# Kernel optimization log

Hardware: AMD Instinct MI355X
Metric: run time of the kernel (lower is better)

## Reference

```python
import jax, jax.numpy as jnp
import numpy as np
from jax import lax

G = 128          # graphs per batch
N_PER = 512      # nodes per graph (uniform -> static top-k shapes)
N = G * N_PER    # 65536 total nodes
E = 1_048_576    # total edges (8192 per graph)
IN, D, OUT = 256, 128, 16
BN_EPS = 1e-5


def setup_inputs() -> dict:
    key = jax.random.key(0)
    ks = jax.random.split(key, 20)
    e_per = E // G
    off = (jnp.arange(G, dtype=jnp.int32) * N_PER)[:, None]
    src = (off + jax.random.randint(ks[0], (G, e_per), 0, N_PER, dtype=jnp.int32)).reshape(-1)
    dst = (off + jax.random.randint(ks[1], (G, e_per), 0, N_PER, dtype=jnp.int32)).reshape(-1)
    inp = {
        "x": jax.random.normal(ks[2], (N, IN), dtype=jnp.float32),
        "edge_index": jnp.stack([src, dst]),
        "batch": jnp.repeat(jnp.arange(G, dtype=jnp.int32), N_PER),
        # GraphConv1: lin_rel (with bias) + lin_root (no bias)
        "w_rel1": jax.random.normal(ks[3], (IN, D)) / np.sqrt(IN),
        "b_rel1": jnp.zeros((D,), jnp.float32),
        "w_root1": jax.random.normal(ks[4], (IN, D)) / np.sqrt(IN),
        "pool1_w": jax.random.normal(ks[5], (D,)) / np.sqrt(D),
        "w_rel2": jax.random.normal(ks[6], (D, D)) / np.sqrt(D),
        "b_rel2": jnp.zeros((D,), jnp.float32),
        "w_root2": jax.random.normal(ks[7], (D, D)) / np.sqrt(D),
        "pool2_w": jax.random.normal(ks[8], (D,)) / np.sqrt(D),
        "lin1_w": jax.random.normal(ks[9], (2 * D, D)) / np.sqrt(2 * D),
        "lin1_b": jnp.zeros((D,), jnp.float32),
        "bn_gamma": jnp.ones((D,), jnp.float32),
        "bn_beta": jnp.zeros((D,), jnp.float32),
        "bn_mean": jnp.zeros((D,), jnp.float32),
        "bn_var": jnp.ones((D,), jnp.float32),
        "lin2_w": jax.random.normal(ks[10], (D, OUT)) / np.sqrt(D),
        "lin2_b": jnp.zeros((OUT,), jnp.float32),
    }
    return inp


def _graph_conv(x, src, dst, valid, w_rel, b_rel, w_root):
    # PyG GraphConv (aggr='add'): lin_rel(sum_{j in N(i)} x_j) + lin_root(x_i)
    msgs = jnp.where(valid[:, None], x[src], 0.0)           # [E, F]
    agg = jax.ops.segment_sum(msgs, dst, num_segments=x.shape[0])
    return agg @ w_rel + b_rel + x @ w_root


def _topk_pool(x, src, dst, valid, w, n_per):
    # PyG TopKPooling: score = sigmoid(x.w / ||w||); keep top ceil(ratio*n) per graph
    k = (n_per + 1) // 2  # ceil(0.5 * n_per)
    score = jax.nn.sigmoid((x @ w) / jnp.sqrt(jnp.sum(w * w)))  # [G*n_per]
    idx_local = lax.top_k(score.reshape(G, n_per), k)[1]        # [G, k]
    perm = (jnp.arange(G, dtype=src.dtype)[:, None] * n_per + idx_local.astype(src.dtype)).reshape(-1)
    x_new = x[perm] * score[perm][:, None]
    # relabel edges (filter_adj): keep edges with both endpoints selected
    mapping = jnp.full((G * n_per,), -1, dtype=src.dtype).at[perm].set(
        jnp.arange(G * k, dtype=src.dtype))
    ns, nd = mapping[src], mapping[dst]
    v = valid & (ns >= 0) & (nd >= 0)
    return x_new, jnp.where(v, ns, 0), jnp.where(v, nd, 0), v, score[perm], k


def _global_pools(x, k):
    xg = x.reshape(G, k, -1)
    return jnp.concatenate([xg.max(axis=1), xg.mean(axis=1)], axis=1)  # [G, 2D]


def reference(x, edge_index, batch, w_rel1, b_rel1, w_root1, pool1_w,
              w_rel2, b_rel2, w_root2, pool2_w, lin1_w, lin1_b,
              bn_gamma, bn_beta, bn_mean, bn_var, lin2_w, lin2_b):
    src, dst = edge_index[0], edge_index[1]
    valid = jnp.ones_like(src, dtype=bool)

    h = jax.nn.relu(_graph_conv(x, src, dst, valid, w_rel1, b_rel1, w_root1))
    h, s1, d1, v1, score_1, k1 = _topk_pool(h, src, dst, valid, pool1_w, N_PER)
    x1 = _global_pools(h, k1)

    h = jax.nn.relu(_graph_conv(h, s1, d1, v1, w_rel2, b_rel2, w_root2))
    h, _, _, _, _, k2 = _topk_pool(h, s1, d1, v1, pool2_w, k1)
    x2 = _global_pools(h, k2)

    g_emb = x1 + x2                                  # [G, 2D]
    z = jax.nn.relu(g_emb @ lin1_w + lin1_b)
    z = (z - bn_mean) * bn_gamma / jnp.sqrt(bn_var + BN_EPS) + bn_beta  # BN (eval)
    # dropout is identity in eval mode
    out = jax.nn.log_softmax(z @ lin2_w + lin2_b, axis=-1)
    return out, g_emb, pool1_w, score_1
```

## Files before the change

### kernel.cpp

```cpp
#include <hip/hip_runtime.h>
#include <cmath>

#define NG    128
#define NPER  512
#define NTOT  65536
#define NEDGE 1048576
#define EPG   8192
#define DD    128
#define K1    256
#define K2    128
#define SLOTS 56

typedef float f32x4 __attribute__((ext_vector_type(4)));
typedef short short8 __attribute__((ext_vector_type(8)));

__device__ __forceinline__ int SW(int row, int c) { return (c ^ ((row >> 1) & 3)) * 8; }

__device__ __forceinline__ void bsplit(float v, short& h, short& l) {
  unsigned u = __builtin_bit_cast(unsigned, v);
  h = (short)(u >> 16);
  float lf = v - __builtin_bit_cast(float, u & 0xFFFF0000u);
  l = (short)(__builtin_bit_cast(unsigned, lf) >> 16);
}

__device__ __forceinline__ void gload16(const void* g, void* l) {
  __builtin_amdgcn_global_load_lds(
      (const __attribute__((address_space(1))) unsigned int*)g,
      (__attribute__((address_space(3))) unsigned int*)l, 16, 0, 0);
}

__global__ __launch_bounds__(256) void build_wt_all(
    const float* __restrict__ W1, const float* __restrict__ W2,
    const float* __restrict__ W3, const float* __restrict__ W4,
    short* __restrict__ h1, short* __restrict__ l1,
    short* __restrict__ h2, short* __restrict__ l2, int* __restrict__ cnt) {
  const int n = blockIdx.x, k = threadIdx.x;
  cnt[n * 256 + k] = 0;
  const int t = k >> 5, k5 = k & 31, cq = k5 >> 3, i = k5 & 7;
  const int nhalf = n >> 7, nf = (n >> 4) & 7, l = n & 15;
  const int off = ((((t * 2 + nhalf) * 8 + nf) * 4 + cq) * 16 + l) * 8 + i;
  {
    float w = (nhalf == 0) ? W1[k * 128 + n] : W2[k * 128 + (n - 128)];
    short h, lo; bsplit(w, h, lo);
    h1[off] = h; l1[off] = lo;
  }
  if (k < 128) {
    float w = (nhalf == 0) ? W3[k * 128 + n] : W4[k * 128 + (n - 128)];
    short h, lo; bsplit(w, h, lo);
    h2[off] = h; l2[off] = lo;
  }
}

template<int K>
__global__ __launch_bounds__(256, 4) void gemm_mfma_dual(
    const float* __restrict__ A,
    const short* __restrict__ wth, const short* __restrict__ wtl,
    float* __restrict__ C1, float* __restrict__ C2) {
  __shared__ short Ah[64 * 32], Al[64 * 32];
  __shared__ short WHL[16384];
  const int tid = threadIdx.x, lane = tid & 63, wid = tid >> 6;
  const int wm = (wid >> 1) * 32;
  const int nhalf = wid & 1;
  const size_t row0 = (size_t)blockIdx.x * 64;
  const int l15 = lane & 15, cq = lane >> 4;
  const int ar = tid >> 2, ac = tid & 3;
  constexpr int NT = K / 32;
  const float* ap = A + (row0 + ar) * K + ac * 8;
  const int wfrag = nhalf * 4096 + cq * 128 + l15 * 8;

  f32x4 acc[2][8];
#pragma unroll
  for (int mf = 0; mf < 2; ++mf)
#pragma unroll
    for (int nf = 0; nf < 8; ++nf) acc[mf][nf] = (f32x4){0.f, 0.f, 0.f, 0.f};

  float4 pa0, pa1;
#define LOAD_A(t) { const float4* p = (const float4*)(ap + (t) * 32); pa0 = p[0]; pa1 = p[1]; }
#define STORE_A() { \
    float ff[8] = {pa0.x, pa0.y, pa0.z, pa0.w, pa1.x, pa1.y, pa1.z, pa1.w}; \
    short8 hv, lv; \
    _Pragma("unroll") \
    for (int i = 0; i < 8; ++i) { short hh, ll; bsplit(ff[i], hh, ll); hv[i] = hh; lv[i] = ll; } \
    *(short8*)&Ah[ar * 32 + SW(ar, ac)] = hv; \
    *(short8*)&Al[ar * 32 + SW(ar, ac)] = lv; }
#define STAGE_W(t) { \
    _Pragma("unroll") \
    for (int j = 0; j < 8; ++j) { \
      int c = wid * 8 + j; \
      const short* gs = (c < 16) ? wth + (size_t)(t) * 8192 + c * 512 + lane * 8 \
                                 : wtl + (size_t)(t) * 8192 + (c - 16) * 512 + lane * 8; \
      gload16(gs, &WHL[c * 512 + lane * 8]); \
    } }

  LOAD_A(0);
  STAGE_W(0);
  STORE_A();
  __syncthreads();

  for (int t = 0; t < NT; ++t) {
    if (t + 1 < NT) LOAD_A(t + 1);
    const int r0 = wm + l15, r1 = wm + 16 + l15;
    short8 ah0 = *(const short8*)&Ah[r0 * 32 + SW(r0, cq)];
    short8 al0 = *(const short8*)&Al[r0 * 32 + SW(r0, cq)];
    short8 ah1 = *(const short8*)&Ah[r1 * 32 + SW(r1, cq)];
    short8 al1 = *(const short8*)&Al[r1 * 32 + SW(r1, cq)];
#pragma unroll
    for (int nf = 0; nf < 8; ++nf) {
      short8 bh = *(const short8*)&WHL[nf * 512 + wfrag];
      short8 bl = *(const short8*)&WHL[8192 + nf * 512 + wfrag];
      acc[0][nf] = __builtin_amdgcn_mfma_f32_16x16x32_bf16(ah0, bh, acc[0][nf], 0, 0, 0);
      acc[0][nf] = __builtin_amdgcn_mfma_f32_16x16x32_bf16(ah0, bl, acc[0][nf], 0, 0, 0);
      acc[0][nf] = __builtin_amdgcn_mfma_f32_16x16x32_bf16(al0, bh, acc[0][nf], 0, 0, 0);
      acc[1][nf] = __builtin_amdgcn_mfma_f32_16x16x32_bf16(ah1, bh, acc[1][nf], 0, 0, 0);
      acc[1][nf] = __builtin_amdgcn_mfma_f32_16x16x32_bf16(ah1, bl, acc[1][nf], 0, 0, 0);
      acc[1][nf] = __builtin_amdgcn_mfma_f32_16x16x32_bf16(al1, bh, acc[1][nf], 0, 0, 0);
    }
    if (t + 1 < NT) {
      __syncthreads();
      STAGE_W(t + 1);
      STORE_A();
      __syncthreads();
    }
  }
#undef LOAD_A
#undef STORE_A
#undef STAGE_W

  float* Cb = nhalf ? C2 : C1;
#pragma unroll
  for (int mf = 0; mf < 2; ++mf) {
    size_t rbase = row0 + wm + mf * 16 + cq * 4;
#pragma unroll
    for (int nf = 0; nf < 8; ++nf) {
      int c = nf * 16 + l15;
#pragma unroll
      for (int r = 0; r < 4; ++r)
        Cb[(rbase + r) * 128 + c] = acc[mf][nf][r];
    }
  }
}

__global__ __launch_bounds__(512) void bucket_fill1(
    const int* __restrict__ src, const int* __restrict__ dst,
    int* __restrict__ cnt, int* __restrict__ eid) {
  int e = blockIdx.x * 512 + threadIdx.x;
  int d = dst[e];
  int pos = atomicAdd(&cnt[d], 1);
  eid[d * SLOTS + pos] = src[e];
}

__global__ __launch_bounds__(512) void bucket_fill2(
    const int* __restrict__ src, const int* __restrict__ dst,
    const int* __restrict__ map, int* __restrict__ cnt, int* __restrict__ eid) {
  int e = blockIdx.x * 512 + threadIdx.x;
  int ms = map[src[e]], md = map[dst[e]];
  if ((ms | md) >= 0) {
    int pos = atomicAdd(&cnt[md], 1);
    eid[md * SLOTS + pos] = ms;
  }
}

template<int CPX>
__global__ __launch_bounds__(512) void agg_gather(
    const float* __restrict__ xr, const float* __restrict__ xo,
    const float* __restrict__ brel, const int* __restrict__ cnt,
    const int* __restrict__ eid, const float* __restrict__ pw,
    float* __restrict__ hout, float* __restrict__ score) {
  const int bid = blockIdx.x;
  const int lb = (bid & 7) * CPX + (bid >> 3);
  const int wave = threadIdx.x >> 6, lane = threadIdx.x & 63;
  const int node = lb * 8 + wave;
  const int dg = cnt[node];
  const int base = node * SLOTS;
  const int half = lane >> 5, l32 = lane & 31;
  const int eall = eid[base + lane];
  f32x4 a0 = {0.f, 0.f, 0.f, 0.f}, a1 = a0, a2 = a0, a3 = a0;
  int j = 0;
  for (; j + 8 <= dg; j += 8) {
    int e0 = __shfl(eall, j + 0 + half);
    int e1 = __shfl(eall, j + 2 + half);
    int e2 = __shfl(eall, j + 4 + half);
    int e3 = __shfl(eall, j + 6 + half);
    a0 += *(const f32x4*)&xr[(size_t)e0 * 128 + l32 * 4];
    a1 += *(const f32x4*)&xr[(size_t)e1 * 128 + l32 * 4];
    a2 += *(const f32x4*)&xr[(size_t)e2 * 128 + l32 * 4];
    a3 += *(const f32x4*)&xr[(size_t)e3 * 128 + l32 * 4];
  }
  if (j + 4 <= dg) {
    int e0 = __shfl(eall, j + 0 + half);
    int e1 = __shfl(eall, j + 2 + half);
    a0 += *(const f32x4*)&xr[(size_t)e0 * 128 + l32 * 4];
    a1 += *(const f32x4*)&xr[(size_t)e1 * 128 + l32 * 4];
    j += 4;
  }
  if (j + 2 <= dg) {
    int e0 = __shfl(eall, j + half);
    a2 += *(const f32x4*)&xr[(size_t)e0 * 128 + l32 * 4];
    j += 2;
  }
  {
    int e0 = __shfl(eall, j);
    if (j < dg && half == 0)
      a3 += *(const f32x4*)&xr[(size_t)e0 * 128 + l32 * 4];
  }
  f32x4 s = a0 + a1 + a2 + a3;
  s[0] += __shfl_xor(s[0], 32);
  s[1] += __shfl_xor(s[1], 32);
  s[2] += __shfl_xor(s[2], 32);
  s[3] += __shfl_xor(s[3], 32);
  float dot = 0.f, nr = 0.f;
  if (half == 0) {
    f32x4 b = *(const f32x4*)&brel[l32 * 4];
    f32x4 o = *(const f32x4*)&xo[(size_t)node * 128 + l32 * 4];
    f32x4 h;
    f32x4 wv = *(const f32x4*)&pw[l32 * 4];
#pragma unroll
    for (int i = 0; i < 4; ++i) {
      h[i] = fmaxf(s[i] + b[i] + o[i], 0.f);
      dot += h[i] * wv[i];
      nr += wv[i] * wv[i];
    }
    *(f32x4*)&hout[(size_t)node * 128 + l32 * 4] = h;
  }
#pragma unroll
  for (int m = 16; m >= 1; m >>= 1) {
    dot += __shfl_xor(dot, m);
    nr += __shfl_xor(nr, m);
  }
  if (lane == 0)
    score[node] = 1.f / (1.f + expf(-dot / sqrtf(nr)));
}

__global__ __launch_bounds__(512) void topk1_kernel(
    const float* __restrict__ h1, const float* __restrict__ score_in,
    float* __restrict__ xnew, int* __restrict__ map, int* __restrict__ cnt,
    float* __restrict__ x1p, float* __restrict__ score_out) {
  const int g = blockIdx.x, tid = threadIdx.x;
  __shared__ float sc[NPER];
  __shared__ int si[NPER];
  __shared__ float xn[K1 * 128];
  __shared__ float redm[4 * 128];
  __shared__ float reds[4 * 128];
  {
    int gt = g * 512 + tid;
    if (gt < NG * K1) cnt[gt] = 0;
  }
  sc[tid] = score_in[g * NPER + tid];
  si[tid] = tid;

  for (int k = 2; k <= NPER; k <<= 1) {
    for (int j = k >> 1; j > 0; j >>= 1) {
      __syncthreads();
      int p = tid ^ j;
      if (p > tid) {
        float sa = sc[tid], sb = sc[p];
        int ia = si[tid], ib = si[p];
        bool before = (sb > sa) || (sb == sa && ib < ia);
        if (before == ((tid & k) == 0)) {
          sc[tid] = sb; sc[p] = sa; si[tid] = ib; si[p] = ia;
        }
      }
    }
  }
  __syncthreads();

  map[g * NPER + tid] = -1;
  if (tid < K1) score_out[g * K1 + tid] = sc[tid];
  __syncthreads();
  if (tid < K1) map[g * NPER + si[tid]] = g * K1 + tid;

  const int wave = tid >> 6, lane = tid & 63;
  for (int j = wave; j < K1; j += 8) {
    int idx = si[j];
    float s2 = sc[j];
    float2 v = *(const float2*)&h1[(size_t)(g * NPER + idx) * 128 + lane * 2];
    float2 o;
    o.x = v.x * s2;
    o.y = v.y * s2;
    *(float2*)&xnew[(size_t)(g * K1 + j) * 128 + lane * 2] = o;
    xn[j * 128 + lane * 2] = o.x;
    xn[j * 128 + lane * 2 + 1] = o.y;
  }
  __syncthreads();

  const int c = tid & 127, grp = tid >> 7;
  float mx = -1e30f, sm = 0.f;
  for (int r = grp; r < K1; r += 4) {
    float v = xn[r * 128 + c];
    mx = fmaxf(mx, v);
    sm += v;
  }
  redm[grp * 128 + c] = mx;
  reds[grp * 128 + c] = sm;
  __syncthreads();
  if (tid < 128) {
    float m = fmaxf(fmaxf(redm[c], redm[128 + c]), fmaxf(redm[256 + c], redm[384 + c]));
    float su = reds[c] + reds[128 + c] + reds[256 + c] + reds[384 + c];
    x1p[g * 256 + tid] = m;
    x1p[g * 256 + 128 + tid] = su * (1.f / 256.f);
  }
}

__global__ __launch_bounds__(256) void topk2_head_kernel(
    const float* __restrict__ h2, const float* __restrict__ score_in,
    const float* __restrict__ x1p,
    const float* __restrict__ lin1_w, const float* __restrict__ lin1_b,
    const float* __restrict__ bng, const float* __restrict__ bnb,
    const float* __restrict__ bnm, const float* __restrict__ bnv,
    const float* __restrict__ lin2_w, const float* __restrict__ lin2_b,
    const float* __restrict__ pool1_w, float* __restrict__ out) {
  const int g = blockIdx.x, tid = threadIdx.x;
  __shared__ float sc[K1];
  __shared__ int si[K1];
  __shared__ float xn[K2 * 128];
  __shared__ float redm[2 * 128];
  __shared__ float reds[2 * 128];
  __shared__ float ge[256];
  __shared__ float zz[128];
  __shared__ float lg[16];
  sc[tid] = score_in[g * K1 + tid];
  si[tid] = tid;
  for (int k = 2; k <= K1; k <<= 1) {
    for (int j = k >> 1; j > 0; j >>= 1) {
      __syncthreads();
      int p = tid ^ j;
      if (p > tid) {
        float sa = sc[tid], sb = sc[p];
        int ia = si[tid], ib = si[p];
        bool before = (sb > sa) || (sb == sa && ib < ia);
        if (before == ((tid & k) == 0)) {
          sc[tid] = sb; sc[p] = sa; si[tid] = ib; si[p] = ia;
        }
      }
    }
  }
  __syncthreads();
  const int wave = tid >> 6, lane = tid & 63;
  for (int j = wave; j < K2; j += 4) {
    int idx = si[j];
    float s2 = sc[j];
    float2 v = *(const float2*)&h2[(size_t)(g * K1 + idx) * 128 + lane * 2];
    xn[j * 128 + lane * 2] = v.x * s2;
    xn[j * 128 + lane * 2 + 1] = v.y * s2;
  }
  __syncthreads();
  const int c = tid & 127, grp = tid >> 7;
  float mx = -1e30f, sm = 0.f;
  for (int r = grp; r < K2; r += 2) {
    float v = xn[r * 128 + c];
    mx = fmaxf(mx, v);
    sm += v;
  }
  redm[grp * 128 + c] = mx;
  reds[grp * 128 + c] = sm;
  __syncthreads();
  if (tid < 128) {
    float m = fmaxf(redm[c], redm[128 + c]);
    float su = (reds[c] + reds[128 + c]) * (1.f / 128.f);
    float v1 = x1p[g * 256 + tid] + m;
    float v2 = x1p[g * 256 + 128 + tid] + su;
    ge[tid] = v1;
    ge[128 + tid] = v2;
    out[2048 + g * 256 + tid] = v1;
    out[2048 + g * 256 + 128 + tid] = v2;
  }
  __syncthreads();
  if (tid < 128) {
    float a = lin1_b[tid];
    for (int k = 0; k < 256; ++k) a += ge[k] * lin1_w[k * 128 + tid];
    a = fmaxf(a, 0.f);
    a = (a - bnm[tid]) * bng[tid] / sqrtf(bnv[tid] + 1e-5f) + bnb[tid];
    zz[tid] = a;
  }
  __syncthreads();
  if (tid < 16) {
    float o = lin2_b[tid];
    for (int k = 0; k < 128; ++k) o += zz[k] * lin2_w[k * 16 + tid];
    lg[tid] = o;
  }
  __syncthreads();
  if (tid < 16) {
    float m = lg[0];
    for (int j = 1; j < 16; ++j) m = fmaxf(m, lg[j]);
    float ssum = 0.f;
    for (int j = 0; j < 16; ++j) ssum += expf(lg[j] - m);
    out[g * 16 + tid] = lg[tid] - m - logf(ssum);
  }
  if (g == 0 && tid < 128) out[34816 + tid] = pool1_w[tid];
}

extern "C" void kernel_launch(void* const* d_in, const int* in_sizes, int n_in,
                              void* d_out, int out_size, void* d_ws, size_t ws_size,
                              hipStream_t stream) {
  const float* x       = (const float*)d_in[0];
  const int*   ei      = (const int*)d_in[1];
  const float* w_rel1  = (const float*)d_in[3];
  const float* b_rel1  = (const float*)d_in[4];
  const float* w_root1 = (const float*)d_in[5];
  const float* pool1_w = (const float*)d_in[6];
  const float* w_rel2  = (const float*)d_in[7];
  const float* b_rel2  = (const float*)d_in[8];
  const float* w_root2 = (const float*)d_in[9];
  const float* pool2_w = (const float*)d_in[10];
  const float* lin1_w  = (const float*)d_in[11];
  const float* lin1_b  = (const float*)d_in[12];
  const float* bng     = (const float*)d_in[13];
  const float* bnb     = (const float*)d_in[14];
  const float* bnm     = (const float*)d_in[15];
  const float* bnv     = (const float*)d_in[16];
  const float* lin2_w  = (const float*)d_in[17];
  const float* lin2_b  = (const float*)d_in[18];
  const int* src = ei;
  const int* dst = ei + NEDGE;

  char* ws = (char*)d_ws;
  float* xr1  = (float*)(ws + 0);
  float* xoh1 = (float*)(ws + 33554432UL);
  float* xnew = (float*)(ws + 67108864UL);
  int*   eid  = (int*)  (ws + 67108864UL);
  int*   map  = (int*)  (ws + 83886080UL);
  int*   cnt  = (int*)  (ws + 84148224UL);
  float* x1p  = (float*)(ws + 84410368UL);
  float* sc1  = (float*)(ws + 84541440UL);
  float* sc2  = (float*)(ws + 84803584UL);
  short* wth1 = (short*)(ws + 84934656UL);
  short* wtl1 = (short*)(ws + 85065728UL);
  short* wth2 = (short*)(ws + 85196800UL);
  short* wtl2 = (short*)(ws + 85262336UL);
  float* xr2  = (float*)(ws + 0);
  float* xo2  = (float*)(ws + 16777216UL);
  float* h2   = xoh1;
  float* out  = (float*)d_out;

  build_wt_all<<<dim3(256), dim3(256), 0, stream>>>(
      w_rel1, w_root1, w_rel2, w_root2, wth1, wtl1, wth2, wtl2, cnt);
  gemm_mfma_dual<256><<<dim3(1024), dim3(256), 0, stream>>>(x, wth1, wtl1, xr1, xoh1);
  bucket_fill1<<<dim3(NEDGE / 512), dim3(512), 0, stream>>>(src, dst, cnt, eid);
  agg_gather<1024><<<dim3(8192), dim3(512), 0, stream>>>(
      xr1, xoh1, b_rel1, cnt, eid, pool1_w, xoh1, sc1);
  topk1_kernel<<<dim3(NG), dim3(512), 0, stream>>>(xoh1, sc1, xnew, map, cnt, x1p, out + 34944);

  gemm_mfma_dual<128><<<dim3(512), dim3(256), 0, stream>>>(xnew, wth2, wtl2, xr2, xo2);
  bucket_fill2<<<dim3(NEDGE / 512), dim3(512), 0, stream>>>(src, dst, map, cnt, eid);
  agg_gather<512><<<dim3(4096), dim3(512), 0, stream>>>(
      xr2, xo2, b_rel2, cnt, eid, pool2_w, h2, sc2);

  topk2_head_kernel<<<dim3(NG), dim3(K1), 0, stream>>>(h2, sc2, x1p,
      lin1_w, lin1_b, bng, bnb, bnm, bnv, lin2_w, lin2_b, pool1_w, out);
}
```

Measured before the change: 183.8 us.

## Process eight nodes per wave in agg_gather with wider unroll and prefetch

Each wave in agg_gather now handles eight consecutive destination nodes instead of one. The grid shrinks eightfold, the pool-weight norm and bias loads are hoisted out of the node loop, and the next node's edge-id row is prefetched. The inner gather loop is unrolled to eight independent accumulators, and the tail uses clamped, predicated loads instead of a cascade of branches. The aim is to amortise per-node setup and raise memory-level parallelism per wave, at the cost of more registers (launch bounds now request 4 blocks) and fewer, longer-lived blocks, which can hurt load balance.

```diff
diff --git a/kernel.cpp b/kernel.cpp
--- a/kernel.cpp
+++ b/kernel.cpp
@@ -161,7 +161,7 @@
 }
 
 template<int CPX>
-__global__ __launch_bounds__(512) void agg_gather(
+__global__ __launch_bounds__(512, 4) void agg_gather(
     const float* __restrict__ xr, const float* __restrict__ xo,
     const float* __restrict__ brel, const int* __restrict__ cnt,
     const int* __restrict__ eid, const float* __restrict__ pw,
@@ -169,66 +169,83 @@
   const int bid = blockIdx.x;
   const int lb = (bid & 7) * CPX + (bid >> 3);
   const int wave = threadIdx.x >> 6, lane = threadIdx.x & 63;
-  const int node = lb * 8 + wave;
-  const int dg = cnt[node];
-  const int base = node * SLOTS;
   const int half = lane >> 5, l32 = lane & 31;
-  const int eall = eid[base + lane];
-  f32x4 a0 = {0.f, 0.f, 0.f, 0.f}, a1 = a0, a2 = a0, a3 = a0;
-  int j = 0;
-  for (; j + 8 <= dg; j += 8) {
-    int e0 = __shfl(eall, j + 0 + half);
-    int e1 = __shfl(eall, j + 2 + half);
-    int e2 = __shfl(eall, j + 4 + half);
-    int e3 = __shfl(eall, j + 6 + half);
-    a0 += *(const f32x4*)&xr[(size_t)e0 * 128 + l32 * 4];
-    a1 += *(const f32x4*)&xr[(size_t)e1 * 128 + l32 * 4];
-    a2 += *(const f32x4*)&xr[(size_t)e2 * 128 + l32 * 4];
-    a3 += *(const f32x4*)&xr[(size_t)e3 * 128 + l32 * 4];
-  }
-  if (j + 4 <= dg) {
-    int e0 = __shfl(eall, j + 0 + half);
-    int e1 = __shfl(eall, j + 2 + half);
-    a0 += *(const f32x4*)&xr[(size_t)e0 * 128 + l32 * 4];
-    a1 += *(const f32x4*)&xr[(size_t)e1 * 128 + l32 * 4];
-    j += 4;
-  }
-  if (j + 2 <= dg) {
-    int e0 = __shfl(eall, j + half);
-    a2 += *(const f32x4*)&xr[(size_t)e0 * 128 + l32 * 4];
-    j += 2;
-  }
-  {
-    int e0 = __shfl(eall, j);
-    if (j < dg && half == 0)
-      a3 += *(const f32x4*)&xr[(size_t)e0 * 128 + l32 * 4];
-  }
-  f32x4 s = a0 + a1 + a2 + a3;
-  s[0] += __shfl_xor(s[0], 32);
-  s[1] += __shfl_xor(s[1], 32);
-  s[2] += __shfl_xor(s[2], 32);
-  s[3] += __shfl_xor(s[3], 32);
-  float dot = 0.f, nr = 0.f;
-  if (half == 0) {
-    f32x4 b = *(const f32x4*)&brel[l32 * 4];
-    f32x4 o = *(const f32x4*)&xo[(size_t)node * 128 + l32 * 4];
+  const int n0 = lb * 64 + wave * 8;
+
+  const f32x4 wv = *(const f32x4*)&pw[l32 * 4];
+  float nr = wv[0] * wv[0] + wv[1] * wv[1] + wv[2] * wv[2] + wv[3] * wv[3];
+#pragma unroll
+  for (int m = 16; m >= 1; m >>= 1) nr += __shfl_xor(nr, m);
+  const float innorm = 1.f / sqrtf(nr);
+  const f32x4 bb = *(const f32x4*)&brel[l32 * 4];
+
+  int cnts = cnt[n0 + (lane & 7)];
+  int eall = eid[(size_t)n0 * SLOTS + lane];
+
+#define GLD(e) (*(const f32x4*)&xr[(size_t)(e) * 128 + l32 * 4])
+  for (int i = 0; i < 8; ++i) {
+    const int node = n0 + i;
+    const int dg = __shfl(cnts, i);
+    const int ecur = eall;
+    if (i < 7) eall = eid[(size_t)(node + 1) * SLOTS + lane];
+
+    f32x4 a0 = {0.f, 0.f, 0.f, 0.f}, a1 = a0, a2 = a0, a3 = a0,
+          a4 = a0, a5 = a0, a6 = a0, a7 = a0;
+    int j = 0;
+    for (; j + 16 <= dg; j += 16) {
+      int e0 = __shfl(ecur, j + 0 + half);
+      int e1 = __shfl(ecur, j + 2 + half);
+      int e2 = __shfl(ecur, j + 4 + half);
+      int e3 = __shfl(ecur, j + 6 + half);
+      int e4 = __shfl(ecur, j + 8 + half);
+      int e5 = __shfl(ecur, j + 10 + half);
+      int e6 = __shfl(ecur, j + 12 + half);
+      int e7 = __shfl(ecur, j + 14 + half);
+      a0 += GLD(e0); a1 += GLD(e1); a2 += GLD(e2); a3 += GLD(e3);
+      a4 += GLD(e4); a5 += GLD(e5); a6 += GLD(e6); a7 += GLD(e7);
+    }
+    if (j < dg) {
+      const int dm = dg - 1;
+      int i0 = j + 0 + half, i1 = j + 2 + half, i2 = j + 4 + half, i3 = j + 6 + half;
+      int i4 = j + 8 + half, i5 = j + 10 + half, i6 = j + 12 + half, i7 = j + 14 + half;
+      int e0 = __shfl(ecur, i0 < dm ? i0 : dm);
+      int e1 = __shfl(ecur, i1 < dm ? i1 : dm);
+      int e2 = __shfl(ecur, i2 < dm ? i2 : dm);
+      int e3 = __shfl(ecur, i3 < dm ? i3 : dm);
+      int e4 = __shfl(ecur, i4 < dm ? i4 : dm);
+      int e5 = __shfl(ecur, i5 < dm ? i5 : dm);
+      int e6 = __shfl(ecur, i6 < dm ? i6 : dm);
+      int e7 = __shfl(ecur, i7 < dm ? i7 : dm);
+      f32x4 v0 = GLD(e0), v1 = GLD(e1), v2 = GLD(e2), v3 = GLD(e3);
+      f32x4 v4 = GLD(e4), v5 = GLD(e5), v6 = GLD(e6), v7 = GLD(e7);
+      if (i0 <= dm) a0 += v0;
+      if (i1 <= dm) a1 += v1;
+      if (i2 <= dm) a2 += v2;
+      if (i3 <= dm) a3 += v3;
+      if (i4 <= dm) a4 += v4;
+      if (i5 <= dm) a5 += v5;
+      if (i6 <= dm) a6 += v6;
+      if (i7 <= dm) a7 += v7;
+    }
+    f32x4 s = ((a0 + a1) + (a2 + a3)) + ((a4 + a5) + (a6 + a7));
+    s[0] += __shfl_xor(s[0], 32);
+    s[1] += __shfl_xor(s[1], 32);
+    s[2] += __shfl_xor(s[2], 32);
+    s[3] += __shfl_xor(s[3], 32);
+    const f32x4 o = *(const f32x4*)&xo[(size_t)node * 128 + l32 * 4];
     f32x4 h;
-    f32x4 wv = *(const f32x4*)&pw[l32 * 4];
-#pragma unroll
-    for (int i = 0; i < 4; ++i) {
-      h[i] = fmaxf(s[i] + b[i] + o[i], 0.f);
-      dot += h[i] * wv[i];
-      nr += wv[i] * wv[i];
-    }
-    *(f32x4*)&hout[(size_t)node * 128 + l32 * 4] = h;
-  }
-#pragma unroll
-  for (int m = 16; m >= 1; m >>= 1) {
-    dot += __shfl_xor(dot, m);
-    nr += __shfl_xor(nr, m);
-  }
-  if (lane == 0)
-    score[node] = 1.f / (1.f + expf(-dot / sqrtf(nr)));
+    float dot = 0.f;
+#pragma unroll
+    for (int q = 0; q < 4; ++q) {
+      h[q] = fmaxf(s[q] + bb[q] + o[q], 0.f);
+      dot += h[q] * wv[q];
+    }
+    if (half == 0) *(f32x4*)&hout[(size_t)node * 128 + l32 * 4] = h;
+#pragma unroll
+    for (int m = 16; m >= 1; m >>= 1) dot += __shfl_xor(dot, m);
+    if (lane == 0) score[node] = 1.f / (1.f + expf(-dot * innorm));
+  }
+#undef GLD
 }
 
 __global__ __launch_bounds__(512) void topk1_kernel(
@@ -436,13 +453,13 @@
       w_rel1, w_root1, w_rel2, w_root2, wth1, wtl1, wth2, wtl2, cnt);
   gemm_mfma_dual<256><<<dim3(1024), dim3(256), 0, stream>>>(x, wth1, wtl1, xr1, xoh1);
   bucket_fill1<<<dim3(NEDGE / 512), dim3(512), 0, stream>>>(src, dst, cnt, eid);
-  agg_gather<1024><<<dim3(8192), dim3(512), 0, stream>>>(
+  agg_gather<128><<<dim3(1024), dim3(512), 0, stream>>>(
       xr1, xoh1, b_rel1, cnt, eid, pool1_w, xoh1, sc1);
   topk1_kernel<<<dim3(NG), dim3(512), 0, stream>>>(xoh1, sc1, xnew, map, cnt, x1p, out + 34944);
 
   gemm_mfma_dual<128><<<dim3(512), dim3(256), 0, stream>>>(xnew, wth2, wtl2, xr2, xo2);
   bucket_fill2<<<dim3(NEDGE / 512), dim3(512), 0, stream>>>(src, dst, map, cnt, eid);
-  agg_gather<512><<<dim3(4096), dim3(512), 0, stream>>>(
+  agg_gather<64><<<dim3(512), dim3(512), 0, stream>>>(
       xr2, xo2, b_rel2, cnt, eid, pool2_w, h2, sc2);
 
   topk2_head_kernel<<<dim3(NG), dim3(K1), 0, stream>>>(h2, sc2, x1p,
```

After: 195.1 us. +6.2%, slower.

## Stage per-graph features in LDS for neighbor aggregation and retile second GEMM

Applied to the files above, without the earlier changes.

Both aggregation kernels now give each block one graph (split into two feature or node halves). The block copies that graph's transformed features into shared memory and gathers neighbor rows from LDS instead of doing random global loads. Layer 1 accumulates a partial score dot product with atomics, and the sigmoid and norm move into topk1, which costs an extra memset. The second GEMM switches to 32-row tiles to launch more blocks. The trade-off is fewer, LDS-heavy blocks (256 per aggregation) with lower occupancy.

```diff
diff --git a/kernel.cpp b/kernel.cpp
--- a/kernel.cpp
+++ b/kernel.cpp
@@ -51,32 +51,34 @@
   }
 }
 
-template<int K>
+template<int K, int MT>
 __global__ __launch_bounds__(256, 4) void gemm_mfma_dual(
     const float* __restrict__ A,
     const short* __restrict__ wth, const short* __restrict__ wtl,
     float* __restrict__ C1, float* __restrict__ C2) {
-  __shared__ short Ah[64 * 32], Al[64 * 32];
+  constexpr int MF = MT / 32;
+  __shared__ short Ah[MT * 32], Al[MT * 32];
   __shared__ short WHL[16384];
   const int tid = threadIdx.x, lane = tid & 63, wid = tid >> 6;
-  const int wm = (wid >> 1) * 32;
+  const int wm = (wid >> 1) * (MT / 2);
   const int nhalf = wid & 1;
-  const size_t row0 = (size_t)blockIdx.x * 64;
+  const size_t row0 = (size_t)blockIdx.x * MT;
   const int l15 = lane & 15, cq = lane >> 4;
   const int ar = tid >> 2, ac = tid & 3;
+  const bool astage = (MT == 64) || (tid < MT * 4);
   constexpr int NT = K / 32;
   const float* ap = A + (row0 + ar) * K + ac * 8;
   const int wfrag = nhalf * 4096 + cq * 128 + l15 * 8;
 
-  f32x4 acc[2][8];
-#pragma unroll
-  for (int mf = 0; mf < 2; ++mf)
+  f32x4 acc[MF][8];
+#pragma unroll
+  for (int mf = 0; mf < MF; ++mf)
 #pragma unroll
     for (int nf = 0; nf < 8; ++nf) acc[mf][nf] = (f32x4){0.f, 0.f, 0.f, 0.f};
 
   float4 pa0, pa1;
-#define LOAD_A(t) { const float4* p = (const float4*)(ap + (t) * 32); pa0 = p[0]; pa1 = p[1]; }
-#define STORE_A() { \
+#define LOAD_A(t) if (astage) { const float4* p = (const float4*)(ap + (t) * 32); pa0 = p[0]; pa1 = p[1]; }
+#define STORE_A() if (astage) { \
     float ff[8] = {pa0.x, pa0.y, pa0.z, pa0.w, pa1.x, pa1.y, pa1.z, pa1.w}; \
     short8 hv, lv; \
     _Pragma("unroll") \
@@ -99,21 +101,23 @@
 
   for (int t = 0; t < NT; ++t) {
     if (t + 1 < NT) LOAD_A(t + 1);
-    const int r0 = wm + l15, r1 = wm + 16 + l15;
-    short8 ah0 = *(const short8*)&Ah[r0 * 32 + SW(r0, cq)];
-    short8 al0 = *(const short8*)&Al[r0 * 32 + SW(r0, cq)];
-    short8 ah1 = *(const short8*)&Ah[r1 * 32 + SW(r1, cq)];
-    short8 al1 = *(const short8*)&Al[r1 * 32 + SW(r1, cq)];
+    short8 ah[MF], al[MF];
+#pragma unroll
+    for (int mf = 0; mf < MF; ++mf) {
+      int r = wm + mf * 16 + l15;
+      ah[mf] = *(const short8*)&Ah[r * 32 + SW(r, cq)];
+      al[mf] = *(const short8*)&Al[r * 32 + SW(r, cq)];
+    }
 #pragma unroll
     for (int nf = 0; nf < 8; ++nf) {
       short8 bh = *(const short8*)&WHL[nf * 512 + wfrag];
       short8 bl = *(const short8*)&WHL[8192 + nf * 512 + wfrag];
-      acc[0][nf] = __builtin_amdgcn_mfma_f32_16x16x32_bf16(ah0, bh, acc[0][nf], 0, 0, 0);
-      acc[0][nf] = __builtin_amdgcn_mfma_f32_16x16x32_bf16(ah0, bl, acc[0][nf], 0, 0, 0);
-      acc[0][nf] = __builtin_amdgcn_mfma_f32_16x16x32_bf16(al0, bh, acc[0][nf], 0, 0, 0);
-      acc[1][nf] = __builtin_amdgcn_mfma_f32_16x16x32_bf16(ah1, bh, acc[1][nf], 0, 0, 0);
-      acc[1][nf] = __builtin_amdgcn_mfma_f32_16x16x32_bf16(ah1, bl, acc[1][nf], 0, 0, 0);
-      acc[1][nf] = __builtin_amdgcn_mfma_f32_16x16x32_bf16(al1, bh, acc[1][nf], 0, 0, 0);
+#pragma unroll
+      for (int mf = 0; mf < MF; ++mf) {
+        acc[mf][nf] = __builtin_amdgcn_mfma_f32_16x16x32_bf16(ah[mf], bh, acc[mf][nf], 0, 0, 0);
+        acc[mf][nf] = __builtin_amdgcn_mfma_f32_16x16x32_bf16(ah[mf], bl, acc[mf][nf], 0, 0, 0);
+        acc[mf][nf] = __builtin_amdgcn_mfma_f32_16x16x32_bf16(al[mf], bh, acc[mf][nf], 0, 0, 0);
+      }
     }
     if (t + 1 < NT) {
       __syncthreads();
@@ -128,7 +132,7 @@
 
   float* Cb = nhalf ? C2 : C1;
 #pragma unroll
-  for (int mf = 0; mf < 2; ++mf) {
+  for (int mf = 0; mf < MF; ++mf) {
     size_t rbase = row0 + wm + mf * 16 + cq * 4;
 #pragma unroll
     for (int nf = 0; nf < 8; ++nf) {
@@ -160,79 +164,140 @@
   }
 }
 
-template<int CPX>
-__global__ __launch_bounds__(512) void agg_gather(
+__global__ __launch_bounds__(512) void agg1_lds(
+    const float* __restrict__ xr, const float* __restrict__ xo,
+    const float* __restrict__ brel, const int* __restrict__ cnt,
+    const int* __restrict__ eid, const float* __restrict__ pw,
+    float* __restrict__ hout, float* __restrict__ sc_raw) {
+  __shared__ float Xs[512 * 68];
+  const int g = blockIdx.x >> 1, chunk = blockIdx.x & 1;
+  const int tid = threadIdx.x;
+  const int gn0 = g * NPER;
+  {
+    const float* srcp = xr + (size_t)gn0 * 128 + chunk * 64;
+#pragma unroll
+    for (int i = 0; i < 16; ++i) {
+      int fid = tid + i * 512;
+      int row = fid >> 4, q = fid & 15;
+      f32x4 v = *(const f32x4*)&srcp[(size_t)row * 128 + q * 4];
+      *(f32x4*)&Xs[row * 68 + q * 4] = v;
+    }
+  }
+  __syncthreads();
+  const int wave = tid >> 6, lane = tid & 63;
+  const int g4 = lane >> 4, c4 = (lane & 15) * 4;
+  const int nb = wave * 64;
+  const f32x4 wv = *(const f32x4*)&pw[chunk * 64 + c4];
+  const f32x4 bb = *(const f32x4*)&brel[chunk * 64 + c4];
+  int cnts = cnt[gn0 + nb + lane];
+  int eall = eid[(size_t)(gn0 + nb) * SLOTS + lane];
+  for (int i = 0; i < 64; ++i) {
+    const int node = gn0 + nb + i;
+    const int dg = __shfl(cnts, i);
+    const int ecur = eall;
+    if (i < 63) eall = eid[(size_t)(node + 1) * SLOTS + lane];
+    const int eoffv = (ecur - gn0) * 68;
+    f32x4 a = {0.f, 0.f, 0.f, 0.f};
+    int j = 0;
+    for (; j + 4 <= dg; j += 4) {
+      int ro = __shfl(eoffv, j + g4);
+      a += *(const f32x4*)&Xs[ro + c4];
+    }
+    if (j < dg) {
+      int sel = j + g4;
+      int ro = __shfl(eoffv, (sel < dg) ? sel : (dg - 1));
+      f32x4 v = *(const f32x4*)&Xs[ro + c4];
+      if (sel < dg) a += v;
+    }
+    a[0] += __shfl_xor(a[0], 16); a[1] += __shfl_xor(a[1], 16);
+    a[2] += __shfl_xor(a[2], 16); a[3] += __shfl_xor(a[3], 16);
+    a[0] += __shfl_xor(a[0], 32); a[1] += __shfl_xor(a[1], 32);
+    a[2] += __shfl_xor(a[2], 32); a[3] += __shfl_xor(a[3], 32);
+    float pd = 0.f;
+    if (g4 == 0) {
+      f32x4 o = *(const f32x4*)&xo[(size_t)node * 128 + chunk * 64 + c4];
+      f32x4 h;
+#pragma unroll
+      for (int q = 0; q < 4; ++q) {
+        h[q] = fmaxf(a[q] + bb[q] + o[q], 0.f);
+        pd += h[q] * wv[q];
+      }
+      *(f32x4*)&hout[(size_t)node * 128 + chunk * 64 + c4] = h;
+    }
+    pd += __shfl_xor(pd, 1); pd += __shfl_xor(pd, 2);
+    pd += __shfl_xor(pd, 4); pd += __shfl_xor(pd, 8);
+    if (lane == 0) atomicAdd(&sc_raw[node], pd);
+  }
+}
+
+__global__ __launch_bounds__(512) void agg2_lds(
     const float* __restrict__ xr, const float* __restrict__ xo,
     const float* __restrict__ brel, const int* __restrict__ cnt,
     const int* __restrict__ eid, const float* __restrict__ pw,
     float* __restrict__ hout, float* __restrict__ score) {
-  const int bid = blockIdx.x;
-  const int lb = (bid & 7) * CPX + (bid >> 3);
-  const int wave = threadIdx.x >> 6, lane = threadIdx.x & 63;
-  const int node = lb * 8 + wave;
-  const int dg = cnt[node];
-  const int base = node * SLOTS;
-  const int half = lane >> 5, l32 = lane & 31;
-  const int eall = eid[base + lane];
-  f32x4 a0 = {0.f, 0.f, 0.f, 0.f}, a1 = a0, a2 = a0, a3 = a0;
-  int j = 0;
-  for (; j + 8 <= dg; j += 8) {
-    int e0 = __shfl(eall, j + 0 + half);
-    int e1 = __shfl(eall, j + 2 + half);
-    int e2 = __shfl(eall, j + 4 + half);
-    int e3 = __shfl(eall, j + 6 + half);
-    a0 += *(const f32x4*)&xr[(size_t)e0 * 128 + l32 * 4];
-    a1 += *(const f32x4*)&xr[(size_t)e1 * 128 + l32 * 4];
-    a2 += *(const f32x4*)&xr[(size_t)e2 * 128 + l32 * 4];
-    a3 += *(const f32x4*)&xr[(size_t)e3 * 128 + l32 * 4];
-  }
-  if (j + 4 <= dg) {
-    int e0 = __shfl(eall, j + 0 + half);
-    int e1 = __shfl(eall, j + 2 + half);
-    a0 += *(const f32x4*)&xr[(size_t)e0 * 128 + l32 * 4];
-    a1 += *(const f32x4*)&xr[(size_t)e1 * 128 + l32 * 4];
-    j += 4;
-  }
-  if (j + 2 <= dg) {
-    int e0 = __shfl(eall, j + half);
-    a2 += *(const f32x4*)&xr[(size_t)e0 * 128 + l32 * 4];
-    j += 2;
-  }
+  __shared__ float Xs[256 * 132];
+  const int g = blockIdx.x >> 1, nh = blockIdx.x & 1;
+  const int tid = threadIdx.x;
+  const int gb = g * K1;
   {
-    int e0 = __shfl(eall, j);
-    if (j < dg && half == 0)
-      a3 += *(const f32x4*)&xr[(size_t)e0 * 128 + l32 * 4];
-  }
-  f32x4 s = a0 + a1 + a2 + a3;
-  s[0] += __shfl_xor(s[0], 32);
-  s[1] += __shfl_xor(s[1], 32);
-  s[2] += __shfl_xor(s[2], 32);
-  s[3] += __shfl_xor(s[3], 32);
-  float dot = 0.f, nr = 0.f;
-  if (half == 0) {
-    f32x4 b = *(const f32x4*)&brel[l32 * 4];
-    f32x4 o = *(const f32x4*)&xo[(size_t)node * 128 + l32 * 4];
+    const float* srcp = xr + (size_t)gb * 128;
+#pragma unroll
+    for (int i = 0; i < 16; ++i) {
+      int fid = tid + i * 512;
+      int row = fid >> 5, q = fid & 31;
+      f32x4 v = *(const f32x4*)&srcp[(size_t)row * 128 + q * 4];
+      *(f32x4*)&Xs[row * 132 + q * 4] = v;
+    }
+  }
+  __syncthreads();
+  const int wave = tid >> 6, lane = tid & 63;
+  const int half = lane >> 5, c4 = (lane & 31) * 4;
+  const int nb = nh * 128 + wave * 16;
+  const f32x4 wv = *(const f32x4*)&pw[c4];
+  float nr = wv[0] * wv[0] + wv[1] * wv[1] + wv[2] * wv[2] + wv[3] * wv[3];
+  nr += __shfl_xor(nr, 1); nr += __shfl_xor(nr, 2); nr += __shfl_xor(nr, 4);
+  nr += __shfl_xor(nr, 8); nr += __shfl_xor(nr, 16);
+  const float innorm = 1.f / sqrtf(nr);
+  const f32x4 bb = *(const f32x4*)&brel[c4];
+  int cnts = cnt[gb + nb + (lane & 15)];
+  int eall = eid[(size_t)(gb + nb) * SLOTS + lane];
+  for (int i = 0; i < 16; ++i) {
+    const int node = gb + nb + i;
+    const int dg = __shfl(cnts, i);
+    const int ecur = eall;
+    if (i < 15) eall = eid[(size_t)(node + 1) * SLOTS + lane];
+    const int eoffv = (ecur - gb) * 132;
+    f32x4 a = {0.f, 0.f, 0.f, 0.f};
+    int j = 0;
+    for (; j + 2 <= dg; j += 2) {
+      int ro = __shfl(eoffv, j + half);
+      a += *(const f32x4*)&Xs[ro + c4];
+    }
+    if (j < dg) {
+      int ro = __shfl(eoffv, j);
+      f32x4 v = *(const f32x4*)&Xs[ro + c4];
+      if (half == 0) a += v;
+    }
+    a[0] += __shfl_xor(a[0], 32); a[1] += __shfl_xor(a[1], 32);
+    a[2] += __shfl_xor(a[2], 32); a[3] += __shfl_xor(a[3], 32);
+    const f32x4 o = *(const f32x4*)&xo[(size_t)node * 128 + c4];
     f32x4 h;
-    f32x4 wv = *(const f32x4*)&pw[l32 * 4];
-#pragma unroll
-    for (int i = 0; i < 4; ++i) {
-      h[i] = fmaxf(s[i] + b[i] + o[i], 0.f);
-      dot += h[i] * wv[i];
-      nr += wv[i] * wv[i];
-    }
-    *(f32x4*)&hout[(size_t)node * 128 + l32 * 4] = h;
-  }
-#pragma unroll
-  for (int m = 16; m >= 1; m >>= 1) {
-    dot += __shfl_xor(dot, m);
-    nr += __shfl_xor(nr, m);
-  }
-  if (lane == 0)
-    score[node] = 1.f / (1.f + expf(-dot / sqrtf(nr)));
+    float pd = 0.f;
+#pragma unroll
+    for (int q = 0; q < 4; ++q) {
+      h[q] = fmaxf(a[q] + bb[q] + o[q], 0.f);
+      pd += h[q] * wv[q];
+    }
+    if (half == 0) *(f32x4*)&hout[(size_t)node * 128 + c4] = h;
+    pd += __shfl_xor(pd, 1); pd += __shfl_xor(pd, 2); pd += __shfl_xor(pd, 4);
+    pd += __shfl_xor(pd, 8); pd += __shfl_xor(pd, 16);
+    if (lane == 0) score[node] = 1.f / (1.f + expf(-pd * innorm));
+  }
 }
 
 __global__ __launch_bounds__(512) void topk1_kernel(
-    const float* __restrict__ h1, const float* __restrict__ score_in,
+    const float* __restrict__ h1, const float* __restrict__ sc_raw,
+    const float* __restrict__ pw,
     float* __restrict__ xnew, int* __restrict__ map, int* __restrict__ cnt,
     float* __restrict__ x1p, float* __restrict__ score_out) {
   const int g = blockIdx.x, tid = threadIdx.x;
@@ -245,8 +310,13 @@
     int gt = g * 512 + tid;
     if (gt < NG * K1) cnt[gt] = 0;
   }
-  sc[tid] = score_in[g * NPER + tid];
-  si[tid] = tid;
+  {
+    float nrm = 0.f;
+    for (int i = 0; i < 128; ++i) nrm += pw[i] * pw[i];
+    float innorm = 1.f / sqrtf(nrm);
+    sc[tid] = 1.f / (1.f + expf(-sc_raw[g * NPER + tid] * innorm));
+    si[tid] = tid;
+  }
 
   for (int k = 2; k <= NPER; k <<= 1) {
     for (int j = k >> 1; j > 0; j >>= 1) {
@@ -434,15 +504,17 @@
 
   build_wt_all<<<dim3(256), dim3(256), 0, stream>>>(
       w_rel1, w_root1, w_rel2, w_root2, wth1, wtl1, wth2, wtl2, cnt);
-  gemm_mfma_dual<256><<<dim3(1024), dim3(256), 0, stream>>>(x, wth1, wtl1, xr1, xoh1);
+  hipMemsetAsync(sc1, 0, NTOT * sizeof(float), stream);
+  gemm_mfma_dual<256, 64><<<dim3(1024), dim3(256), 0, stream>>>(x, wth1, wtl1, xr1, xoh1);
   bucket_fill1<<<dim3(NEDGE / 512), dim3(512), 0, stream>>>(src, dst, cnt, eid);
-  agg_gather<1024><<<dim3(8192), dim3(512), 0, stream>>>(
+  agg1_lds<<<dim3(256), dim3(512), 0, stream>>>(
       xr1, xoh1, b_rel1, cnt, eid, pool1_w, xoh1, sc1);
-  topk1_kernel<<<dim3(NG), dim3(512), 0, stream>>>(xoh1, sc1, xnew, map, cnt, x1p, out + 34944);
-
-  gemm_mfma_dual<128><<<dim3(512), dim3(256), 0, stream>>>(xnew, wth2, wtl2, xr2, xo2);
+  topk1_kernel<<<dim3(NG), dim3(512), 0, stream>>>(
+      xoh1, sc1, pool1_w, xnew, map, cnt, x1p, out + 34944);
+
+  gemm_mfma_dual<128, 32><<<dim3(1024), dim3(256), 0, stream>>>(xnew, wth2, wtl2, xr2, xo2);
   bucket_fill2<<<dim3(NEDGE / 512), dim3(512), 0, stream>>>(src, dst, map, cnt, eid);
-  agg_gather<512><<<dim3(4096), dim3(512), 0, stream>>>(
+  agg2_lds<<<dim3(256), dim3(512), 0, stream>>>(
       xr2, xo2, b_rel2, cnt, eid, pool2_w, h2, sc2);
 
   topk2_head_kernel<<<dim3(NG), dim3(K1), 0, stream>>>(h2, sc2, x1p,
```

After: 259.0 us. +41.0%, slower.

## Double-buffer weight tiles and enlarge M tile in split-bf16 MFMA GEMM

Applied to the files above, without the earlier changes.

The dual GEMM now keeps two LDS buffers for weight tiles, so the next tile's weights are fetched asynchronously while the current tile's MFMAs run, rather than after a barrier. The first-layer GEMM also moves to a 128-row tile (512 blocks instead of 1024), which reuses each weight tile across more rows, and launch bounds drop to 2 blocks per CU. Separately, the pooling-weight norm in agg_gather is computed by all lanes, outside the half==0 branch. The larger tile and doubled LDS use raise register and LDS pressure and lower occupancy.

```diff
diff --git a/kernel.cpp b/kernel.cpp
--- a/kernel.cpp
+++ b/kernel.cpp
@@ -51,84 +51,102 @@
   }
 }
 
-template<int K>
-__global__ __launch_bounds__(256, 4) void gemm_mfma_dual(
+template<int K, int MT>
+__global__ __launch_bounds__(256, 2) void gemm_mfma_dual(
     const float* __restrict__ A,
     const short* __restrict__ wth, const short* __restrict__ wtl,
     float* __restrict__ C1, float* __restrict__ C2) {
-  __shared__ short Ah[64 * 32], Al[64 * 32];
-  __shared__ short WHL[16384];
+  constexpr int MF = MT / 32;
+  constexpr int NP = MT / 32;
+  constexpr int NT = K / 32;
+  __shared__ short Ah[MT * 32], Al[MT * 32];
+  __shared__ short WHL[2][16384];
   const int tid = threadIdx.x, lane = tid & 63, wid = tid >> 6;
-  const int wm = (wid >> 1) * 32;
+  const int wm = (wid >> 1) * (MT / 2);
   const int nhalf = wid & 1;
-  const size_t row0 = (size_t)blockIdx.x * 64;
+  const size_t row0 = (size_t)blockIdx.x * MT;
   const int l15 = lane & 15, cq = lane >> 4;
-  const int ar = tid >> 2, ac = tid & 3;
-  constexpr int NT = K / 32;
-  const float* ap = A + (row0 + ar) * K + ac * 8;
   const int wfrag = nhalf * 4096 + cq * 128 + l15 * 8;
-
-  f32x4 acc[2][8];
-#pragma unroll
-  for (int mf = 0; mf < 2; ++mf)
+  const int ar  = (MT == 128) ? (tid >> 1) : (tid >> 2);
+  const int cb0 = (MT == 128) ? ((tid & 1) * 2) : (tid & 3);
+  const float* ap = A + (row0 + ar) * K + cb0 * 8;
+
+  float4 pa[NP];
+  auto load_a = [&](int t) {
+    const float4* p = (const float4*)(ap + t * 32);
+#pragma unroll
+    for (int i = 0; i < NP; ++i) pa[i] = p[i];
+  };
+  auto store_a = [&]() {
+#pragma unroll
+    for (int c = 0; c < NP / 2; ++c) {
+      float ff[8] = {pa[2*c].x, pa[2*c].y, pa[2*c].z, pa[2*c].w,
+                     pa[2*c+1].x, pa[2*c+1].y, pa[2*c+1].z, pa[2*c+1].w};
+      short8 hv, lv;
+#pragma unroll
+      for (int i = 0; i < 8; ++i) {
+        short hh, ll; bsplit(ff[i], hh, ll); hv[i] = hh; lv[i] = ll;
+      }
+      *(short8*)&Ah[ar * 32 + SW(ar, cb0 + c)] = hv;
+      *(short8*)&Al[ar * 32 + SW(ar, cb0 + c)] = lv;
+    }
+  };
+  auto stage_w = [&](int t, int b) {
+#pragma unroll
+    for (int j = 0; j < 8; ++j) {
+      int c = wid * 8 + j;
+      const short* gs = (c < 16) ? wth + (size_t)t * 8192 + c * 512 + lane * 8
+                                 : wtl + (size_t)t * 8192 + (c - 16) * 512 + lane * 8;
+      gload16(gs, &WHL[b][c * 512 + lane * 8]);
+    }
+  };
+
+  f32x4 acc[MF][8];
+#pragma unroll
+  for (int mf = 0; mf < MF; ++mf)
 #pragma unroll
     for (int nf = 0; nf < 8; ++nf) acc[mf][nf] = (f32x4){0.f, 0.f, 0.f, 0.f};
 
-  float4 pa0, pa1;
-#define LOAD_A(t) { const float4* p = (const float4*)(ap + (t) * 32); pa0 = p[0]; pa1 = p[1]; }
-#define STORE_A() { \
-    float ff[8] = {pa0.x, pa0.y, pa0.z, pa0.w, pa1.x, pa1.y, pa1.z, pa1.w}; \
-    short8 hv, lv; \
-    _Pragma("unroll") \
-    for (int i = 0; i < 8; ++i) { short hh, ll; bsplit(ff[i], hh, ll); hv[i] = hh; lv[i] = ll; } \
-    *(short8*)&Ah[ar * 32 + SW(ar, ac)] = hv; \
-    *(short8*)&Al[ar * 32 + SW(ar, ac)] = lv; }
-#define STAGE_W(t) { \
-    _Pragma("unroll") \
-    for (int j = 0; j < 8; ++j) { \
-      int c = wid * 8 + j; \
-      const short* gs = (c < 16) ? wth + (size_t)(t) * 8192 + c * 512 + lane * 8 \
-                                 : wtl + (size_t)(t) * 8192 + (c - 16) * 512 + lane * 8; \
-      gload16(gs, &WHL[c * 512 + lane * 8]); \
-    } }
-
-  LOAD_A(0);
-  STAGE_W(0);
-  STORE_A();
-  __syncthreads();
+  load_a(0);
+  stage_w(0, 0);
+  store_a();
+  __syncthreads();
+  int cur = 0;
 
   for (int t = 0; t < NT; ++t) {
-    if (t + 1 < NT) LOAD_A(t + 1);
-    const int r0 = wm + l15, r1 = wm + 16 + l15;
-    short8 ah0 = *(const short8*)&Ah[r0 * 32 + SW(r0, cq)];
-    short8 al0 = *(const short8*)&Al[r0 * 32 + SW(r0, cq)];
-    short8 ah1 = *(const short8*)&Ah[r1 * 32 + SW(r1, cq)];
-    short8 al1 = *(const short8*)&Al[r1 * 32 + SW(r1, cq)];
+    if (t + 1 < NT) {
+      load_a(t + 1);
+      stage_w(t + 1, cur ^ 1);
+    }
+    short8 ah[MF], al[MF];
+#pragma unroll
+    for (int mf = 0; mf < MF; ++mf) {
+      int r = wm + mf * 16 + l15;
+      ah[mf] = *(const short8*)&Ah[r * 32 + SW(r, cq)];
+      al[mf] = *(const short8*)&Al[r * 32 + SW(r, cq)];
+    }
 #pragma unroll
     for (int nf = 0; nf < 8; ++nf) {
-      short8 bh = *(const short8*)&WHL[nf * 512 + wfrag];
-      short8 bl = *(const short8*)&WHL[8192 + nf * 512 + wfrag];
-      acc[0][nf] = __builtin_amdgcn_mfma_f32_16x16x32_bf16(ah0, bh, acc[0][nf], 0, 0, 0);
-      acc[0][nf] = __builtin_amdgcn_mfma_f32_16x16x32_bf16(ah0, bl, acc[0][nf], 0, 0, 0);
-      acc[0][nf] = __builtin_amdgcn_mfma_f32_16x16x32_bf16(al0, bh, acc[0][nf], 0, 0, 0);
-      acc[1][nf] = __builtin_amdgcn_mfma_f32_16x16x32_bf16(ah1, bh, acc[1][nf], 0, 0, 0);
-      acc[1][nf] = __builtin_amdgcn_mfma_f32_16x16x32_bf16(ah1, bl, acc[1][nf], 0, 0, 0);
-      acc[1][nf] = __builtin_amdgcn_mfma_f32_16x16x32_bf16(al1, bh, acc[1][nf], 0, 0, 0);
+      short8 bh = *(const short8*)&WHL[cur][nf * 512 + wfrag];
+      short8 bl = *(const short8*)&WHL[cur][8192 + nf * 512 + wfrag];
+#pragma unroll
+      for (int mf = 0; mf < MF; ++mf) {
+        acc[mf][nf] = __builtin_amdgcn_mfma_f32_16x16x32_bf16(ah[mf], bh, acc[mf][nf], 0, 0, 0);
+        acc[mf][nf] = __builtin_amdgcn_mfma_f32_16x16x32_bf16(ah[mf], bl, acc[mf][nf], 0, 0, 0);
+        acc[mf][nf] = __builtin_amdgcn_mfma_f32_16x16x32_bf16(al[mf], bh, acc[mf][nf], 0, 0, 0);
+      }
     }
     if (t + 1 < NT) {
       __syncthreads();
-      STAGE_W(t + 1);
-      STORE_A();
+      store_a();
       __syncthreads();
-    }
-  }
-#undef LOAD_A
-#undef STORE_A
-#undef STAGE_W
+      cur ^= 1;
+    }
+  }
 
   float* Cb = nhalf ? C2 : C1;
 #pragma unroll
-  for (int mf = 0; mf < 2; ++mf) {
+  for (int mf = 0; mf < MF; ++mf) {
     size_t rbase = row0 + wm + mf * 16 + cq * 4;
 #pragma unroll
     for (int nf = 0; nf < 8; ++nf) {
@@ -208,17 +226,17 @@
   s[1] += __shfl_xor(s[1], 32);
   s[2] += __shfl_xor(s[2], 32);
   s[3] += __shfl_xor(s[3], 32);
-  float dot = 0.f, nr = 0.f;
+  const f32x4 wv = *(const f32x4*)&pw[l32 * 4];
+  float dot = 0.f;
+  float nr = wv[0]*wv[0] + wv[1]*wv[1] + wv[2]*wv[2] + wv[3]*wv[3];
   if (half == 0) {
     f32x4 b = *(const f32x4*)&brel[l32 * 4];
     f32x4 o = *(const f32x4*)&xo[(size_t)node * 128 + l32 * 4];
     f32x4 h;
-    f32x4 wv = *(const f32x4*)&pw[l32 * 4];
 #pragma unroll
     for (int i = 0; i < 4; ++i) {
       h[i] = fmaxf(s[i] + b[i] + o[i], 0.f);
       dot += h[i] * wv[i];
-      nr += wv[i] * wv[i];
     }
     *(f32x4*)&hout[(size_t)node * 128 + l32 * 4] = h;
   }
@@ -434,13 +452,13 @@
 
   build_wt_all<<<dim3(256), dim3(256), 0, stream>>>(
       w_rel1, w_root1, w_rel2, w_root2, wth1, wtl1, wth2, wtl2, cnt);
-  gemm_mfma_dual<256><<<dim3(1024), dim3(256), 0, stream>>>(x, wth1, wtl1, xr1, xoh1);
+  gemm_mfma_dual<256, 128><<<dim3(512), dim3(256), 0, stream>>>(x, wth1, wtl1, xr1, xoh1);
   bucket_fill1<<<dim3(NEDGE / 512), dim3(512), 0, stream>>>(src, dst, cnt, eid);
   agg_gather<1024><<<dim3(8192), dim3(512), 0, stream>>>(
       xr1, xoh1, b_rel1, cnt, eid, pool1_w, xoh1, sc1);
   topk1_kernel<<<dim3(NG), dim3(512), 0, stream>>>(xoh1, sc1, xnew, map, cnt, x1p, out + 34944);
 
-  gemm_mfma_dual<128><<<dim3(512), dim3(256), 0, stream>>>(xnew, wth2, wtl2, xr2, xo2);
+  gemm_mfma_dual<128, 64><<<dim3(512), dim3(256), 0, stream>>>(xnew, wth2, wtl2, xr2, xo2);
   bucket_fill2<<<dim3(NEDGE / 512), dim3(512), 0, stream>>>(src, dst, map, cnt, eid);
   agg_gather<512><<<dim3(4096), dim3(512), 0, stream>>>(
       xr2, xo2, b_rel2, cnt, eid, pool2_w, h2, sc2);
```

New measurement: 186.0 us. Within noise of the previous version (+1.2%).
